# Kernel tuning notes

Hardware: AMD Instinct MI355X
Metric: run time of the kernel (lower is better)

Reference implementation:

```python
import jax, jax.numpy as jnp
import numpy as np
import random

NQUBIT = 4
NUM_CIRCUITS = 3
SEED = 1024
C64 = jnp.complex64

SINGLE = ['rx', 'ry', 'rz', 's', 't', 'p', 'u3']
DOUBLE = ['rxx', 'ryy', 'rzz', 'swap', 'cnot', 'cp', 'ch', 'cu', 'ct', 'cz']
PCOUNT = {'rx': 1, 'ry': 1, 'rz': 1, 's': 0, 't': 0, 'p': 1, 'u3': 3,
          'rxx': 1, 'ryy': 1, 'rzz': 1, 'swap': 0, 'cnot': 0, 'cp': 1,
          'ch': 0, 'cu': 3, 'ct': 0, 'cz': 0}


def build_circuits(nqubit=NQUBIT, num_circuits=NUM_CIRCUITS, seed=SEED):
    # Replays the torch module's python `random` stream (random.seed(seed))
    rng = random.Random(seed)
    circuits, off = [], 0
    for _ in range(num_circuits):
        gates = []
        for _blk in range(3):
            for i in range(nqubit):
                g = rng.choice(SINGLE)
                gates.append((g, (i,), off, PCOUNT[g])); off += PCOUNT[g]
            c, t = rng.sample(range(0, nqubit - 1), 2)
            g = rng.choice(DOUBLE)
            gates.append((g, (c, t), off, PCOUNT[g])); off += PCOUNT[g]
        circuits.append(gates)
    return circuits, off


def u3mat(th, ph, lam):
    c = jnp.cos(th * 0.5).astype(C64)
    s = jnp.sin(th * 0.5).astype(C64)
    eip = jnp.exp(1j * ph.astype(C64))
    eil = jnp.exp(1j * lam.astype(C64))
    return jnp.stack([jnp.stack([c, -eil * s]), jnp.stack([eip * s, eip * eil * c])])


def mat1(name, p):
    if name == 's':
        return jnp.array([[1, 0], [0, 1j]], C64)
    if name == 't':
        return jnp.array([[1, 0], [0, np.exp(1j * np.pi / 4)]], C64)
    if name == 'u3':
        return u3mat(p[0], p[1], p[2])
    one = jnp.ones((), C64); zero = jnp.zeros((), C64)
    if name == 'p':
        return jnp.stack([jnp.stack([one, zero]), jnp.stack([zero, jnp.exp(1j * p[0].astype(C64))])])
    h = p[0] * 0.5
    if name == 'rx':
        c = jnp.cos(h).astype(C64); s = (-1j * jnp.sin(h)).astype(C64)
        return jnp.stack([jnp.stack([c, s]), jnp.stack([s, c])])
    if name == 'ry':
        c = jnp.cos(h).astype(C64); s = jnp.sin(h).astype(C64)
        return jnp.stack([jnp.stack([c, -s]), jnp.stack([s, c])])
    if name == 'rz':
        e = jnp.exp(-1j * h.astype(C64))
        return jnp.stack([jnp.stack([e, zero]), jnp.stack([zero, jnp.conj(e)])])
    raise ValueError(name)


def mat2(name, p):
    if name == 'swap':
        return jnp.array([[1, 0, 0, 0], [0, 0, 1, 0], [0, 1, 0, 0], [0, 0, 0, 1]], C64)
    if name == 'cnot':
        return jnp.array([[1, 0, 0, 0], [0, 1, 0, 0], [0, 0, 0, 1], [0, 0, 1, 0]], C64)
    if name == 'cz':
        return jnp.diag(jnp.array([1, 1, 1, -1], C64))
    if name == 'ct':
        return jnp.diag(jnp.array([1, 1, 1, np.exp(1j * np.pi / 4)], C64))
    if name == 'ch':
        m = np.eye(4, dtype=np.complex64); r = 1.0 / np.sqrt(2.0)
        m[2:, 2:] = [[r, r], [r, -r]]
        return jnp.asarray(m)
    if name == 'cp':
        one = jnp.ones((), C64)
        return jnp.diag(jnp.stack([one, one, one, jnp.exp(1j * p[0].astype(C64))]))
    if name == 'cu':
        return jnp.zeros((4, 4), C64).at[:2, :2].set(jnp.eye(2, dtype=C64)).at[2:, 2:].set(u3mat(p[0], p[1], p[2]))
    h = p[0] * 0.5
    if name == 'rzz':
        e = jnp.exp(-1j * h.astype(C64)); ec = jnp.conj(e)
        return jnp.diag(jnp.stack([e, ec, ec, e]))
    if name == 'rxx':
        c = jnp.cos(h).astype(C64); s = (-1j * jnp.sin(h)).astype(C64)
        XX = jnp.array([[0, 0, 0, 1], [0, 0, 1, 0], [0, 1, 0, 0], [1, 0, 0, 0]], C64)
        return c * jnp.eye(4, dtype=C64) + s * XX
    if name == 'ryy':
        c = jnp.cos(h).astype(C64); s = (1j * jnp.sin(h)).astype(C64)
        YY = jnp.array([[0, 0, 0, 1], [0, 0, -1, 0], [0, -1, 0, 0], [1, 0, 0, 0]], C64)
        return c * jnp.eye(4, dtype=C64) + s * YY
    raise ValueError(name)


def apply1(state, U, q):
    # state: (N, 2,2,2,2); contract qubit-q axis with U
    state = jnp.moveaxis(state, 1 + q, -1)
    state = state @ U.T
    return jnp.moveaxis(state, -1, 1 + q)


def apply2(state, U, q0, q1):
    state = jnp.moveaxis(state, (1 + q0, 1 + q1), (-2, -1))
    sh = state.shape
    state = (state.reshape(sh[:-2] + (4,)) @ U.T).reshape(sh)
    return jnp.moveaxis(state, (-2, -1), (1 + q0, 1 + q1))


def zsigns(nqubit):
    idx = np.arange(2 ** nqubit)
    return np.stack([1.0 - 2.0 * ((idx >> (nqubit - 1 - q)) & 1) for q in range(nqubit)]).astype(np.float32)


def run_circuit(angles, params, gates, nqubit):
    N = angles.shape[0]
    h = angles * 0.5
    # rx(angle)|0> = [cos(a/2), -i sin(a/2)] per qubit -> product state (encode layer)
    v = jnp.stack([jnp.cos(h), -1j * jnp.sin(h)], axis=-1).astype(C64)  # (N, nq, 2)
    state = jnp.ones((N,), C64)
    for i in range(nqubit):
        state = state[..., None] * v[:, i].reshape((N,) + (1,) * i + (2,))
    for (name, qs, off, cnt) in gates:
        p = params[off:off + cnt]
        if len(qs) == 1:
            state = apply1(state, mat1(name, p), qs[0])
        else:
            state = apply2(state, mat2(name, p), qs[0], qs[1])
    probs = (state.real ** 2 + state.imag ** 2).reshape(N, -1)
    return probs @ jnp.asarray(zsigns(nqubit)).T  # (N, nqubit) Pauli-Z expectations


def _forward(x, params):
    B, C, H, W = x.shape
    circuits, _ = build_circuits()
    x_unf = jnp.moveaxis(x.reshape(B, C, H // 2, 2, W), 3, 4)  # torch unfold(2, 2, 2)
    xr = x_unf.reshape(-1, NQUBIT)
    exps = [run_circuit(xr, params, g, NQUBIT) for g in circuits]
    return jnp.stack(exps, axis=1).reshape(B, NUM_CIRCUITS, W, W)


def setup_inputs():
    key = jax.random.key(0)
    k1, k2 = jax.random.split(key)
    x = jax.random.normal(k1, (512, 1, 64, 64), jnp.float32)
    _, nparams = build_circuits()
    params = jax.random.uniform(k2, (nparams,), jnp.float32, -np.pi, np.pi)
    return {"x": x, "params": params}


def reference(x, params):
    return _forward(x, params)
```

## Files before the change

kernel.cpp:

```cpp
#include <hip/hip_runtime.h>
#include <stdint.h>


namespace {

typedef _Float16 half8 __attribute__((ext_vector_type(8)));
typedef _Float16 half4 __attribute__((ext_vector_type(4)));
typedef float float4v __attribute__((ext_vector_type(4)));

struct GateList {
  int ty[45];
  int q0[45];
  int q1[45];
  int off[45];
};

struct PyRandom {
  uint32_t mt[624];
  int mti;
  void init_genrand(uint32_t s) {
    mt[0] = s;
    for (int i = 1; i < 624; ++i)
      mt[i] = 1812433253u * (mt[i - 1] ^ (mt[i - 1] >> 30)) + (uint32_t)i;
    mti = 624;
  }
  void init_by_array(const uint32_t* key, int klen) {
    init_genrand(19650218u);
    int i = 1, j = 0;
    int k = 624 > klen ? 624 : klen;
    for (; k; --k) {
      mt[i] = (mt[i] ^ ((mt[i - 1] ^ (mt[i - 1] >> 30)) * 1664525u)) + key[j] + (uint32_t)j;
      ++i; ++j;
      if (i >= 624) { mt[0] = mt[623]; i = 1; }
      if (j >= klen) j = 0;
    }
    for (k = 623; k; --k) {
      mt[i] = (mt[i] ^ ((mt[i - 1] ^ (mt[i - 1] >> 30)) * 1566083941u)) - (uint32_t)i;
      ++i;
      if (i >= 624) { mt[0] = mt[623]; i = 1; }
    }
    mt[0] = 0x80000000u;
    mti = 624;
  }
  uint32_t genrand() {
    if (mti >= 624) {
      const uint32_t mag[2] = {0u, 0x9908b0dfu};
      int kk; uint32_t y;
      for (kk = 0; kk < 227; ++kk) {
        y = (mt[kk] & 0x80000000u) | (mt[kk + 1] & 0x7fffffffu);
        mt[kk] = mt[kk + 397] ^ (y >> 1) ^ mag[y & 1];
      }
      for (; kk < 623; ++kk) {
        y = (mt[kk] & 0x80000000u) | (mt[kk + 1] & 0x7fffffffu);
        mt[kk] = mt[kk - 227] ^ (y >> 1) ^ mag[y & 1];
      }
      y = (mt[623] & 0x80000000u) | (mt[0] & 0x7fffffffu);
      mt[623] = mt[396] ^ (y >> 1) ^ mag[y & 1];
      mti = 0;
    }
    uint32_t y = mt[mti++];
    y ^= y >> 11;
    y ^= (y << 7) & 0x9d2c5680u;
    y ^= (y << 15) & 0xefc60000u;
    y ^= y >> 18;
    return y;
  }
  uint32_t getrandbits(int k) { return genrand() >> (32 - k); }
  uint32_t randbelow(uint32_t n) {
    int k = 32 - __builtin_clz(n);
    uint32_t r = getrandbits(k);
    while (r >= n) r = getrandbits(k);
    return r;
  }
};

void build_gatelist(GateList& gl) {
  PyRandom rng;
  uint32_t key = 1024u;
  rng.init_by_array(&key, 1);
  static const int PC_S[7]  = {1, 1, 1, 0, 0, 1, 3};
  static const int PC_D[10] = {1, 1, 1, 0, 0, 1, 0, 3, 0, 0};
  int off = 0, idx = 0;
  for (int circ = 0; circ < 3; ++circ) {
    for (int blk = 0; blk < 3; ++blk) {
      for (int i = 0; i < 4; ++i) {
        int g = (int)rng.randbelow(7);
        gl.ty[idx] = g; gl.q0[idx] = i; gl.q1[idx] = 0; gl.off[idx] = off;
        off += PC_S[g]; ++idx;
      }
      int pool[3] = {0, 1, 2};
      int j0 = (int)rng.randbelow(3); int c = pool[j0]; pool[j0] = pool[2];
      int j1 = (int)rng.randbelow(2); int t = pool[j1];
      int g = (int)rng.randbelow(10);
      gl.ty[idx] = 10 + g; gl.q0[idx] = c; gl.q1[idx] = t; gl.off[idx] = off;
      off += PC_D[g]; ++idx;
    }
  }
}

__device__ inline float2 cmul(float2 a, float2 b) {
  return make_float2(a.x * b.x - a.y * b.y, a.x * b.y + a.y * b.x);
}
__device__ inline float2 cadd(float2 a, float2 b) {
  return make_float2(a.x + b.x, a.y + b.y);
}
__device__ inline float2 shflx(float2 v, int m) {
  return make_float2(__shfl_xor(v.x, m), __shfl_xor(v.y, m));
}

__global__ __launch_bounds__(768) void build_T(
    const float* __restrict__ params, _Float16* __restrict__ Tws, GateList gl) {
  __shared__ float2 ldsU[768];
  __shared__ float  ldsA[3072];

  const int tid = threadIdx.x;

  ((uint64_t*)Tws)[tid] = 0ull;

  {
    const int circ = tid >> 8;
    const int col  = (tid >> 4) & 15;
    const int k    = tid & 15;

    float2 s = make_float2(k == col ? 1.f : 0.f, 0.f);

    for (int g = 0; g < 15; ++g) {
      int gi = circ * 15 + g;
      int ty = gl.ty[gi];
      int o  = gl.off[gi];
      if (ty < 7) {
        float2 G00 = make_float2(1, 0), G01 = make_float2(0, 0),
               G10 = make_float2(0, 0), G11 = make_float2(1, 0);
        if (ty == 0) {
          float c, sn; __sincosf(params[o] * 0.5f, &sn, &c);
          G00 = make_float2(c, 0); G01 = make_float2(0, -sn);
          G10 = make_float2(0, -sn); G11 = make_float2(c, 0);
        } else if (ty == 1) {
          float c, sn; __sincosf(params[o] * 0.5f, &sn, &c);
          G00 = make_float2(c, 0); G01 = make_float2(-sn, 0);
          G10 = make_float2(sn, 0); G11 = make_float2(c, 0);
        } else if (ty == 2) {
          float c, sn; __sincosf(params[o] * 0.5f, &sn, &c);
          G00 = make_float2(c, -sn); G11 = make_float2(c, sn);
        } else if (ty == 3) {
          G11 = make_float2(0, 1);
        } else if (ty == 4) {
          G11 = make_float2(0.7071067811865476f, 0.7071067811865476f);
        } else if (ty == 5) {
          float cp, sp; __sincosf(params[o], &sp, &cp);
          G11 = make_float2(cp, sp);
        } else {
          float th = params[o], phv = params[o + 1], lm = params[o + 2];
          float c, sn; __sincosf(th * 0.5f, &sn, &c);
          float cp, sp; __sincosf(phv, &sp, &cp);
          float cl, sl; __sincosf(lm, &sl, &cl);
          G00 = make_float2(c, 0);
          G01 = make_float2(-cl * sn, -sl * sn);
          G10 = make_float2(cp * sn, sp * sn);
          G11 = make_float2((cp * cl - sp * sl) * c, (cp * sl + sp * cl) * c);
        }
        int m = 1 << (3 - gl.q0[gi]);
        bool hib = (k & m) != 0;
        float2 p = shflx(s, m);
        float2 A = hib ? G11 : G00;
        float2 B = hib ? G10 : G01;
        s = cadd(cmul(A, s), cmul(B, p));
      } else {
        float2 G[4][4];
#pragma unroll
        for (int r2 = 0; r2 < 4; ++r2)
#pragma unroll
          for (int c2 = 0; c2 < 4; ++c2) G[r2][c2] = make_float2(0, 0);
        if (ty == 10) {
          float c, sn; __sincosf(params[o] * 0.5f, &sn, &c);
          G[0][0] = G[1][1] = G[2][2] = G[3][3] = make_float2(c, 0);
          G[0][3] = G[1][2] = G[2][1] = G[3][0] = make_float2(0, -sn);
        } else if (ty == 11) {
          float c, sn; __sincosf(params[o] * 0.5f, &sn, &c);
          G[0][0] = G[1][1] = G[2][2] = G[3][3] = make_float2(c, 0);
          G[0][3] = G[3][0] = make_float2(0, sn);
          G[1][2] = G[2][1] = make_float2(0, -sn);
        } else if (ty == 12) {
          float c, sn; __sincosf(params[o] * 0.5f, &sn, &c);
          G[0][0] = G[3][3] = make_float2(c, -sn);
          G[1][1] = G[2][2] = make_float2(c, sn);
        } else if (ty == 13) {
          G[0][0] = make_float2(1, 0); G[1][2] = make_float2(1, 0);
          G[2][1] = make_float2(1, 0); G[3][3] = make_float2(1, 0);
        } else if (ty == 14) {
          G[0][0] = G[1][1] = make_float2(1, 0);
          G[2][3] = G[3][2] = make_float2(1, 0);
        } else if (ty == 15) {
          G[0][0] = G[1][1] = G[2][2] = make_float2(1, 0);
          float cp, sp; __sincosf(params[o], &sp, &cp);
          G[3][3] = make_float2(cp, sp);
        } else if (ty == 16) {
          G[0][0] = G[1][1] = make_float2(1, 0);
          float rv = 0.7071067811865476f;
          G[2][2] = make_float2(rv, 0); G[2][3] = make_float2(rv, 0);
          G[3][2] = make_float2(rv, 0); G[3][3] = make_float2(-rv, 0);
        } else if (ty == 17) {
          G[0][0] = G[1][1] = make_float2(1, 0);
          float th = params[o], phv = params[o + 1], lm = params[o + 2];
          float c, sn; __sincosf(th * 0.5f, &sn, &c);
          float cp, sp; __sincosf(phv, &sp, &cp);
          float cl, sl; __sincosf(lm, &sl, &cl);
          G[2][2] = make_float2(c, 0);
          G[2][3] = make_float2(-cl * sn, -sl * sn);
          G[3][2] = make_float2(cp * sn, sp * sn);
          G[3][3] = make_float2((cp * cl - sp * sl) * c, (cp * sl + sp * cl) * c);
        } else if (ty == 18) {
          G[0][0] = G[1][1] = G[2][2] = make_float2(1, 0);
          G[3][3] = make_float2(0.7071067811865476f, 0.7071067811865476f);
        } else {
          G[0][0] = G[1][1] = G[2][2] = make_float2(1, 0);
          G[3][3] = make_float2(-1, 0);
        }
        int m0 = 1 << (3 - gl.q0[gi]);
        int m1 = 1 << (3 - gl.q1[gi]);
        bool b0 = (k & m0) != 0;
        bool b1 = (k & m1) != 0;
        float2 p0 = s;
        float2 p1 = shflx(s, m1);
        float2 p2 = shflx(s, m0);
        float2 p3 = shflx(s, m0 ^ m1);
        float2 acc = make_float2(0, 0);
#pragma unroll
        for (int jj = 0; jj < 4; ++jj) {
          float2 r0 = b1 ? G[1][1 ^ jj] : G[0][0 ^ jj];
          float2 r1 = b1 ? G[3][3 ^ jj] : G[2][2 ^ jj];
          float2 coef = b0 ? r1 : r0;
          float2 pj = (jj == 0) ? p0 : (jj == 1) ? p1 : (jj == 2) ? p2 : p3;
          acc = cadd(acc, cmul(coef, pj));
        }
        s = acc;
      }
    }

    int pc = __popc(col) & 3;
    float2 ph = make_float2(1, 0);
    if (pc == 1) ph = make_float2(0, -1);
    else if (pc == 2) ph = make_float2(-1, 0);
    else if (pc == 3) ph = make_float2(0, 1);
    float2 v = cmul(s, ph);

    ldsU[(circ * 16 + k) * 16 + col] = v;
  }
  __syncthreads();

  {
    const int circ = tid >> 8;
    const int k    = (tid >> 4) & 15;
    const int l    = tid & 15;
    float a0 = 0.f, a1 = 0.f, a2 = 0.f, a3 = 0.f;
#pragma unroll
    for (int i = 0; i < 16; ++i) {
      float2 uk = ldsU[(circ * 16 + i) * 16 + k];
      float2 ul = ldsU[(circ * 16 + i) * 16 + l];
      float t = uk.x * ul.x + uk.y * ul.y;
      a0 += (i & 8) ? -t : t;
      a1 += (i & 4) ? -t : t;
      a2 += (i & 2) ? -t : t;
      a3 += (i & 1) ? -t : t;
    }
    ldsA[((circ * 4 + 0) * 16 + k) * 16 + l] = a0;
    ldsA[((circ * 4 + 1) * 16 + k) * 16 + l] = a1;
    ldsA[((circ * 4 + 2) * 16 + k) * 16 + l] = a2;
    ldsA[((circ * 4 + 3) * 16 + k) * 16 + l] = a3;
  }
  __syncthreads();

  for (int idx = tid; idx < 1152; idx += 768) {
    int cq = idx / 96;
    int K  = idx - cq * 96;
    int mf = K >> 5, r = K & 31;
    if (r >= 27) continue;
    int jarr[4] = {mf, r / 9, (r / 3) % 3, r % 3};
    float acc = 0.f;
    for (int sel = 0; sel < 16; ++sel) {
      int kk = 0, ll = 0;
      float sg = 1.f;
#pragma unroll
      for (int q = 0; q < 4; ++q) {
        int t = (sel >> (3 - q)) & 1;
        kk |= t << (3 - q);
        int lb = (jarr[q] == 2) ? (1 - t) : t;
        ll |= lb << (3 - q);
        if (jarr[q] == 1 && t) sg = -sg;
      }
      acc += sg * ldsA[(cq * 16 + kk) * 16 + ll];
    }
    float T = acc * 0.0625f;
    _Float16 th = (_Float16)T;
    _Float16 tl = (_Float16)(T - (float)th);
    int L  = ((r >> 3) << 4) | cq;
    int jj = r & 7;
    Tws[((mf * 2 + 0) * 64 + L) * 8 + jj] = th;
    Tws[((mf * 2 + 1) * 64 + L) * 8 + jj] = tl;
  }
}

__global__ __launch_bounds__(256, 4) void qconv_main(
    const float* __restrict__ x, const _Float16* __restrict__ T,
    float* __restrict__ out) {
  __shared__ _Float16 lds[256 * 40];
  const int tid  = threadIdx.x;
  const int wid  = tid >> 6;
  const int lane = tid & 63;
  const int quad = lane >> 4;
  const int n16  = lane & 15;
  const int r = blockIdx.x * 256 + tid;

  const int b  = r >> 10;
  const int h2 = (r >> 5) & 31;
  const int j  = r & 31;
  const float* xb = x + b * 4096 + h2 * 128 + j * 2;
  float2 lo = *(const float2*)(xb);
  float2 hi = *(const float2*)(xb + 64);
  float c0, s0, c1, s1, c2, s2, c3, s3;
  __sincosf(lo.x, &s0, &c0);
  __sincosf(hi.x, &s1, &c1);
  __sincosf(lo.y, &s2, &c2);
  __sincosf(hi.y, &s3, &c3);

  float f1a[3] = {1.f, c1, s1};
  float f23[9];
  {
    float f2a[3] = {1.f, c2, s2}, f3a[3] = {1.f, c3, s3};
#pragma unroll
    for (int a = 0; a < 9; ++a) f23[a] = f2a[a / 3] * f3a[a % 3];
  }
  __align__(16) _Float16 gh[32];
#pragma unroll
  for (int r1 = 0; r1 < 3; ++r1)
#pragma unroll
    for (int b9 = 0; b9 < 9; ++b9)
      gh[r1 * 9 + b9] = (_Float16)(f1a[r1] * f23[b9]);
#pragma unroll
  for (int e = 27; e < 32; ++e) gh[e] = (_Float16)0.f;

  {
    half8* dst = (half8*)&lds[tid * 40];
    dst[0] = *(const half8*)&gh[0];
    dst[1] = *(const half8*)&gh[8];
    dst[2] = *(const half8*)&gh[16];
    dst[3] = *(const half8*)&gh[24];
    half4 f0h = {(_Float16)1.f, (_Float16)c0, (_Float16)s0, (_Float16)0.f};
    *(half4*)&lds[tid * 40 + 32] = f0h;
  }
  __syncthreads();

  const half8* Tv = (const half8*)T;
  half8 afh[3], afl[3];
#pragma unroll
  for (int mf = 0; mf < 3; ++mf) {
    afh[mf] = Tv[(mf * 2 + 0) * 64 + lane];
    afl[mf] = Tv[(mf * 2 + 1) * 64 + lane];
  }

  half8 slice[4];
  half4 f0v[4];
#pragma unroll
  for (int t = 0; t < 4; ++t) {
    const int row = wid * 64 + t * 16 + n16;
    slice[t] = *(const half8*)&lds[row * 40 + quad * 8];
    f0v[t]   = *(const half4*)&lds[row * 40 + 32];
  }

  float4v acc[4];
#pragma unroll
  for (int t = 0; t < 4; ++t) acc[t] = (float4v){0.f, 0.f, 0.f, 0.f};
#pragma unroll
  for (int mf = 0; mf < 3; ++mf) {
#pragma unroll
    for (int t = 0; t < 4; ++t) {
      _Float16 f0s = f0v[t][mf];
      half8 bf;
#pragma unroll
      for (int e = 0; e < 8; ++e) bf[e] = slice[t][e] * f0s;
      acc[t] = __builtin_amdgcn_mfma_f32_16x16x32_f16(afl[mf], bf, acc[t], 0, 0, 0);
      acc[t] = __builtin_amdgcn_mfma_f32_16x16x32_f16(afh[mf], bf, acc[t], 0, 0, 0);
    }
  }

  if (quad < 3) {
#pragma unroll
    for (int t = 0; t < 4; ++t) {
      int rowg = blockIdx.x * 256 + wid * 64 + t * 16 + n16;
      float4v ev = acc[t];
      __builtin_nontemporal_store(ev, (float4v*)(out + (size_t)rowg * 12 + quad * 4));
    }
  }
}

}

extern "C" void kernel_launch(void* const* d_in, const int* in_sizes, int n_in,
                              void* d_out, int out_size, void* d_ws, size_t ws_size,
                              hipStream_t stream) {
  const float* x      = (const float*)d_in[0];
  const float* params = (const float*)d_in[1];
  float* out = (float*)d_out;
  _Float16* Tws = (_Float16*)d_ws;

  GateList gl;
  build_gatelist(gl);

  hipLaunchKernelGGL(build_T, dim3(1), dim3(768), 0, stream, params, Tws, gl);

  int nrows = in_sizes[0] / 4;
  int grid  = nrows / 256;
  hipLaunchKernelGGL(qconv_main, dim3(grid), dim3(256), 0, stream,
                     x, Tws, out);
}
```

Baseline: 80.63 us.

## Fuse transfer-matrix build into main kernel, recomputing per block in LDS

Removes the separate single-block build_T launch and its global workspace round-trip. Each block of the fused kernel rebuilds the per-circuit transfer matrix in shared memory, prefetching its x inputs before the build, then runs the MFMA contraction over 1024 rows in two passes. The LDS layout for the input features is XOR-swizzled to reduce bank conflicts. The cost is redundant matrix construction in all 512 blocks and a larger shared-memory footprint per block, which may limit occupancy.

```diff
diff --git a/kernel.cpp b/kernel.cpp
--- a/kernel.cpp
+++ b/kernel.cpp
@@ -108,169 +108,197 @@
   return make_float2(__shfl_xor(v.x, m), __shfl_xor(v.y, m));
 }
 
-__global__ __launch_bounds__(768) void build_T(
-    const float* __restrict__ params, _Float16* __restrict__ Tws, GateList gl) {
-  __shared__ float2 ldsU[768];
-  __shared__ float  ldsA[3072];
+__global__ __launch_bounds__(512, 4) void qconv_fused(
+    const float* __restrict__ x, const float* __restrict__ params,
+    float* __restrict__ out, GateList gl, int nP) {
+  __shared__ __align__(16) char smem[47104];
+  _Float16* ldsG = (_Float16*)smem;
+  float2*   ldsU = (float2*)smem;
+  float*    ldsA = (float*)(smem + 6144);
+  float*    ldsP = (float*)(smem + 18432);
+  _Float16* ldsT = (_Float16*)(smem + 40960);
 
   const int tid = threadIdx.x;
-
-  ((uint64_t*)Tws)[tid] = 0ull;
+  const int bid = blockIdx.x;
 
   {
-    const int circ = tid >> 8;
-    const int col  = (tid >> 4) & 15;
-    const int k    = tid & 15;
-
-    float2 s = make_float2(k == col ? 1.f : 0.f, 0.f);
-
-    for (int g = 0; g < 15; ++g) {
-      int gi = circ * 15 + g;
-      int ty = gl.ty[gi];
-      int o  = gl.off[gi];
-      if (ty < 7) {
-        float2 G00 = make_float2(1, 0), G01 = make_float2(0, 0),
-               G10 = make_float2(0, 0), G11 = make_float2(1, 0);
-        if (ty == 0) {
-          float c, sn; __sincosf(params[o] * 0.5f, &sn, &c);
-          G00 = make_float2(c, 0); G01 = make_float2(0, -sn);
-          G10 = make_float2(0, -sn); G11 = make_float2(c, 0);
-        } else if (ty == 1) {
-          float c, sn; __sincosf(params[o] * 0.5f, &sn, &c);
-          G00 = make_float2(c, 0); G01 = make_float2(-sn, 0);
-          G10 = make_float2(sn, 0); G11 = make_float2(c, 0);
-        } else if (ty == 2) {
-          float c, sn; __sincosf(params[o] * 0.5f, &sn, &c);
-          G00 = make_float2(c, -sn); G11 = make_float2(c, sn);
-        } else if (ty == 3) {
-          G11 = make_float2(0, 1);
-        } else if (ty == 4) {
-          G11 = make_float2(0.7071067811865476f, 0.7071067811865476f);
-        } else if (ty == 5) {
-          float cp, sp; __sincosf(params[o], &sp, &cp);
-          G11 = make_float2(cp, sp);
+    uint64_t* z = (uint64_t*)ldsT;
+    for (int i = tid; i < 768; i += 512) z[i] = 0;
+  }
+  for (int i = tid; i < nP; i += 512) ldsP[i] = params[i];
+
+  float2 plo[2], phi[2];
+#pragma unroll
+  for (int t2 = 0; t2 < 2; ++t2) {
+    int r = bid * 1024 + t2 * 512 + tid;
+    const float* xb = x + ((r >> 10) << 12) + (((r >> 5) & 31) << 7) + ((r & 31) << 1);
+    plo[t2] = *(const float2*)(xb);
+    phi[t2] = *(const float2*)(xb + 64);
+  }
+  __syncthreads();
+
+#pragma unroll
+  for (int it = 0; it < 2; ++it) {
+    int s = tid + (it << 9);
+    if (s < 768) {
+      const int circ = __builtin_amdgcn_readfirstlane(s >> 8);
+      const int col  = (s >> 4) & 15;
+      const int k    = s & 15;
+
+      float2 st = make_float2(k == col ? 1.f : 0.f, 0.f);
+
+      for (int g = 0; g < 15; ++g) {
+        int gi = circ * 15 + g;
+        int ty = gl.ty[gi];
+        int o  = gl.off[gi];
+        if (ty < 7) {
+          float2 G00 = make_float2(1, 0), G01 = make_float2(0, 0),
+                 G10 = make_float2(0, 0), G11 = make_float2(1, 0);
+          if (ty == 0) {
+            float c, sn; __sincosf(ldsP[o] * 0.5f, &sn, &c);
+            G00 = make_float2(c, 0); G01 = make_float2(0, -sn);
+            G10 = make_float2(0, -sn); G11 = make_float2(c, 0);
+          } else if (ty == 1) {
+            float c, sn; __sincosf(ldsP[o] * 0.5f, &sn, &c);
+            G00 = make_float2(c, 0); G01 = make_float2(-sn, 0);
+            G10 = make_float2(sn, 0); G11 = make_float2(c, 0);
+          } else if (ty == 2) {
+            float c, sn; __sincosf(ldsP[o] * 0.5f, &sn, &c);
+            G00 = make_float2(c, -sn); G11 = make_float2(c, sn);
+          } else if (ty == 3) {
+            G11 = make_float2(0, 1);
+          } else if (ty == 4) {
+            G11 = make_float2(0.7071067811865476f, 0.7071067811865476f);
+          } else if (ty == 5) {
+            float cp, sp; __sincosf(ldsP[o], &sp, &cp);
+            G11 = make_float2(cp, sp);
+          } else {
+            float th = ldsP[o], phv = ldsP[o + 1], lm = ldsP[o + 2];
+            float c, sn; __sincosf(th * 0.5f, &sn, &c);
+            float cp, sp; __sincosf(phv, &sp, &cp);
+            float cl, sl; __sincosf(lm, &sl, &cl);
+            G00 = make_float2(c, 0);
+            G01 = make_float2(-cl * sn, -sl * sn);
+            G10 = make_float2(cp * sn, sp * sn);
+            G11 = make_float2((cp * cl - sp * sl) * c, (cp * sl + sp * cl) * c);
+          }
+          int m = 1 << (3 - gl.q0[gi]);
+          bool hib = (k & m) != 0;
+          float2 p = shflx(st, m);
+          float2 A = hib ? G11 : G00;
+          float2 B = hib ? G10 : G01;
+          st = cadd(cmul(A, st), cmul(B, p));
         } else {
-          float th = params[o], phv = params[o + 1], lm = params[o + 2];
-          float c, sn; __sincosf(th * 0.5f, &sn, &c);
-          float cp, sp; __sincosf(phv, &sp, &cp);
-          float cl, sl; __sincosf(lm, &sl, &cl);
-          G00 = make_float2(c, 0);
-          G01 = make_float2(-cl * sn, -sl * sn);
-          G10 = make_float2(cp * sn, sp * sn);
-          G11 = make_float2((cp * cl - sp * sl) * c, (cp * sl + sp * cl) * c);
+          float2 G[4][4];
+#pragma unroll
+          for (int r2 = 0; r2 < 4; ++r2)
+#pragma unroll
+            for (int c2 = 0; c2 < 4; ++c2) G[r2][c2] = make_float2(0, 0);
+          if (ty == 10) {
+            float c, sn; __sincosf(ldsP[o] * 0.5f, &sn, &c);
+            G[0][0] = G[1][1] = G[2][2] = G[3][3] = make_float2(c, 0);
+            G[0][3] = G[1][2] = G[2][1] = G[3][0] = make_float2(0, -sn);
+          } else if (ty == 11) {
+            float c, sn; __sincosf(ldsP[o] * 0.5f, &sn, &c);
+            G[0][0] = G[1][1] = G[2][2] = G[3][3] = make_float2(c, 0);
+            G[0][3] = G[3][0] = make_float2(0, sn);
+            G[1][2] = G[2][1] = make_float2(0, -sn);
+          } else if (ty == 12) {
+            float c, sn; __sincosf(ldsP[o] * 0.5f, &sn, &c);
+            G[0][0] = G[3][3] = make_float2(c, -sn);
+            G[1][1] = G[2][2] = make_float2(c, sn);
+          } else if (ty == 13) {
+            G[0][0] = make_float2(1, 0); G[1][2] = make_float2(1, 0);
+            G[2][1] = make_float2(1, 0); G[3][3] = make_float2(1, 0);
+          } else if (ty == 14) {
+            G[0][0] = G[1][1] = make_float2(1, 0);
+            G[2][3] = G[3][2] = make_float2(1, 0);
+          } else if (ty == 15) {
+            G[0][0] = G[1][1] = G[2][2] = make_float2(1, 0);
+            float cp, sp; __sincosf(ldsP[o], &sp, &cp);
+            G[3][3] = make_float2(cp, sp);
+          } else if (ty == 16) {
+            G[0][0] = G[1][1] = make_float2(1, 0);
+            float rv = 0.7071067811865476f;
+            G[2][2] = make_float2(rv, 0); G[2][3] = make_float2(rv, 0);
+            G[3][2] = make_float2(rv, 0); G[3][3] = make_float2(-rv, 0);
+          } else if (ty == 17) {
+            G[0][0] = G[1][1] = make_float2(1, 0);
+            float th = ldsP[o], phv = ldsP[o + 1], lm = ldsP[o + 2];
+            float c, sn; __sincosf(th * 0.5f, &sn, &c);
+            float cp, sp; __sincosf(phv, &sp, &cp);
+            float cl, sl; __sincosf(lm, &sl, &cl);
+            G[2][2] = make_float2(c, 0);
+            G[2][3] = make_float2(-cl * sn, -sl * sn);
+            G[3][2] = make_float2(cp * sn, sp * sn);
+            G[3][3] = make_float2((cp * cl - sp * sl) * c, (cp * sl + sp * cl) * c);
+          } else if (ty == 18) {
+            G[0][0] = G[1][1] = G[2][2] = make_float2(1, 0);
+            G[3][3] = make_float2(0.7071067811865476f, 0.7071067811865476f);
+          } else {
+            G[0][0] = G[1][1] = G[2][2] = make_float2(1, 0);
+            G[3][3] = make_float2(-1, 0);
+          }
+          int m0 = 1 << (3 - gl.q0[gi]);
+          int m1 = 1 << (3 - gl.q1[gi]);
+          bool b0 = (k & m0) != 0;
+          bool b1 = (k & m1) != 0;
+          float2 p0 = st;
+          float2 p1 = shflx(st, m1);
+          float2 p2 = shflx(st, m0);
+          float2 p3 = shflx(st, m0 ^ m1);
+          float2 acc = make_float2(0, 0);
+#pragma unroll
+          for (int jj = 0; jj < 4; ++jj) {
+            float2 r0 = b1 ? G[1][1 ^ jj] : G[0][0 ^ jj];
+            float2 r1 = b1 ? G[3][3 ^ jj] : G[2][2 ^ jj];
+            float2 coef = b0 ? r1 : r0;
+            float2 pj = (jj == 0) ? p0 : (jj == 1) ? p1 : (jj == 2) ? p2 : p3;
+            acc = cadd(acc, cmul(coef, pj));
+          }
+          st = acc;
         }
-        int m = 1 << (3 - gl.q0[gi]);
-        bool hib = (k & m) != 0;
-        float2 p = shflx(s, m);
-        float2 A = hib ? G11 : G00;
-        float2 B = hib ? G10 : G01;
-        s = cadd(cmul(A, s), cmul(B, p));
-      } else {
-        float2 G[4][4];
-#pragma unroll
-        for (int r2 = 0; r2 < 4; ++r2)
-#pragma unroll
-          for (int c2 = 0; c2 < 4; ++c2) G[r2][c2] = make_float2(0, 0);
-        if (ty == 10) {
-          float c, sn; __sincosf(params[o] * 0.5f, &sn, &c);
-          G[0][0] = G[1][1] = G[2][2] = G[3][3] = make_float2(c, 0);
-          G[0][3] = G[1][2] = G[2][1] = G[3][0] = make_float2(0, -sn);
-        } else if (ty == 11) {
-          float c, sn; __sincosf(params[o] * 0.5f, &sn, &c);
-          G[0][0] = G[1][1] = G[2][2] = G[3][3] = make_float2(c, 0);
-          G[0][3] = G[3][0] = make_float2(0, sn);
-          G[1][2] = G[2][1] = make_float2(0, -sn);
-        } else if (ty == 12) {
-          float c, sn; __sincosf(params[o] * 0.5f, &sn, &c);
-          G[0][0] = G[3][3] = make_float2(c, -sn);
-          G[1][1] = G[2][2] = make_float2(c, sn);
-        } else if (ty == 13) {
-          G[0][0] = make_float2(1, 0); G[1][2] = make_float2(1, 0);
-          G[2][1] = make_float2(1, 0); G[3][3] = make_float2(1, 0);
-        } else if (ty == 14) {
-          G[0][0] = G[1][1] = make_float2(1, 0);
-          G[2][3] = G[3][2] = make_float2(1, 0);
-        } else if (ty == 15) {
-          G[0][0] = G[1][1] = G[2][2] = make_float2(1, 0);
-          float cp, sp; __sincosf(params[o], &sp, &cp);
-          G[3][3] = make_float2(cp, sp);
-        } else if (ty == 16) {
-          G[0][0] = G[1][1] = make_float2(1, 0);
-          float rv = 0.7071067811865476f;
-          G[2][2] = make_float2(rv, 0); G[2][3] = make_float2(rv, 0);
-          G[3][2] = make_float2(rv, 0); G[3][3] = make_float2(-rv, 0);
-        } else if (ty == 17) {
-          G[0][0] = G[1][1] = make_float2(1, 0);
-          float th = params[o], phv = params[o + 1], lm = params[o + 2];
-          float c, sn; __sincosf(th * 0.5f, &sn, &c);
-          float cp, sp; __sincosf(phv, &sp, &cp);
-          float cl, sl; __sincosf(lm, &sl, &cl);
-          G[2][2] = make_float2(c, 0);
-          G[2][3] = make_float2(-cl * sn, -sl * sn);
-          G[3][2] = make_float2(cp * sn, sp * sn);
-          G[3][3] = make_float2((cp * cl - sp * sl) * c, (cp * sl + sp * cl) * c);
-        } else if (ty == 18) {
-          G[0][0] = G[1][1] = G[2][2] = make_float2(1, 0);
-          G[3][3] = make_float2(0.7071067811865476f, 0.7071067811865476f);
-        } else {
-          G[0][0] = G[1][1] = G[2][2] = make_float2(1, 0);
-          G[3][3] = make_float2(-1, 0);
-        }
-        int m0 = 1 << (3 - gl.q0[gi]);
-        int m1 = 1 << (3 - gl.q1[gi]);
-        bool b0 = (k & m0) != 0;
-        bool b1 = (k & m1) != 0;
-        float2 p0 = s;
-        float2 p1 = shflx(s, m1);
-        float2 p2 = shflx(s, m0);
-        float2 p3 = shflx(s, m0 ^ m1);
-        float2 acc = make_float2(0, 0);
-#pragma unroll
-        for (int jj = 0; jj < 4; ++jj) {
-          float2 r0 = b1 ? G[1][1 ^ jj] : G[0][0 ^ jj];
-          float2 r1 = b1 ? G[3][3 ^ jj] : G[2][2 ^ jj];
-          float2 coef = b0 ? r1 : r0;
-          float2 pj = (jj == 0) ? p0 : (jj == 1) ? p1 : (jj == 2) ? p2 : p3;
-          acc = cadd(acc, cmul(coef, pj));
-        }
-        s = acc;
-      }
-    }
-
-    int pc = __popc(col) & 3;
-    float2 ph = make_float2(1, 0);
-    if (pc == 1) ph = make_float2(0, -1);
-    else if (pc == 2) ph = make_float2(-1, 0);
-    else if (pc == 3) ph = make_float2(0, 1);
-    float2 v = cmul(s, ph);
-
-    ldsU[(circ * 16 + k) * 16 + col] = v;
+      }
+
+      int pc = __popc(col) & 3;
+      float2 ph = make_float2(1, 0);
+      if (pc == 1) ph = make_float2(0, -1);
+      else if (pc == 2) ph = make_float2(-1, 0);
+      else if (pc == 3) ph = make_float2(0, 1);
+      float2 v = cmul(st, ph);
+
+      ldsU[(circ * 16 + k) * 16 + col] = v;
+    }
   }
   __syncthreads();
 
-  {
-    const int circ = tid >> 8;
-    const int k    = (tid >> 4) & 15;
-    const int l    = tid & 15;
-    float a0 = 0.f, a1 = 0.f, a2 = 0.f, a3 = 0.f;
-#pragma unroll
-    for (int i = 0; i < 16; ++i) {
-      float2 uk = ldsU[(circ * 16 + i) * 16 + k];
-      float2 ul = ldsU[(circ * 16 + i) * 16 + l];
-      float t = uk.x * ul.x + uk.y * ul.y;
-      a0 += (i & 8) ? -t : t;
-      a1 += (i & 4) ? -t : t;
-      a2 += (i & 2) ? -t : t;
-      a3 += (i & 1) ? -t : t;
-    }
-    ldsA[((circ * 4 + 0) * 16 + k) * 16 + l] = a0;
-    ldsA[((circ * 4 + 1) * 16 + k) * 16 + l] = a1;
-    ldsA[((circ * 4 + 2) * 16 + k) * 16 + l] = a2;
-    ldsA[((circ * 4 + 3) * 16 + k) * 16 + l] = a3;
+#pragma unroll
+  for (int it = 0; it < 2; ++it) {
+    int s = tid + (it << 9);
+    if (s < 768) {
+      const int circ = s >> 8;
+      const int k    = (s >> 4) & 15;
+      const int l    = s & 15;
+      float a0 = 0.f, a1 = 0.f, a2 = 0.f, a3 = 0.f;
+#pragma unroll
+      for (int i = 0; i < 16; ++i) {
+        float2 uk = ldsU[(circ * 16 + i) * 16 + k];
+        float2 ul = ldsU[(circ * 16 + i) * 16 + l];
+        float t = uk.x * ul.x + uk.y * ul.y;
+        a0 += (i & 8) ? -t : t;
+        a1 += (i & 4) ? -t : t;
+        a2 += (i & 2) ? -t : t;
+        a3 += (i & 1) ? -t : t;
+      }
+      ldsA[((circ * 4 + 0) * 16 + k) * 16 + l] = a0;
+      ldsA[((circ * 4 + 1) * 16 + k) * 16 + l] = a1;
+      ldsA[((circ * 4 + 2) * 16 + k) * 16 + l] = a2;
+      ldsA[((circ * 4 + 3) * 16 + k) * 16 + l] = a3;
+    }
   }
   __syncthreads();
 
-  for (int idx = tid; idx < 1152; idx += 768) {
+  for (int idx = tid; idx < 1152; idx += 512) {
     int cq = idx / 96;
     int K  = idx - cq * 96;
     int mf = K >> 5, r = K & 31;
@@ -290,67 +318,22 @@
       }
       acc += sg * ldsA[(cq * 16 + kk) * 16 + ll];
     }
-    float T = acc * 0.0625f;
-    _Float16 th = (_Float16)T;
-    _Float16 tl = (_Float16)(T - (float)th);
+    float Tval = acc * 0.0625f;
+    _Float16 th = (_Float16)Tval;
+    _Float16 tl = (_Float16)(Tval - (float)th);
     int L  = ((r >> 3) << 4) | cq;
     int jj = r & 7;
-    Tws[((mf * 2 + 0) * 64 + L) * 8 + jj] = th;
-    Tws[((mf * 2 + 1) * 64 + L) * 8 + jj] = tl;
-  }
-}
-
-__global__ __launch_bounds__(256, 4) void qconv_main(
-    const float* __restrict__ x, const _Float16* __restrict__ T,
-    float* __restrict__ out) {
-  __shared__ _Float16 lds[256 * 40];
-  const int tid  = threadIdx.x;
+    ldsT[((mf * 2 + 0) * 64 + L) * 8 + jj] = th;
+    ldsT[((mf * 2 + 1) * 64 + L) * 8 + jj] = tl;
+  }
+  __syncthreads();
+
   const int wid  = tid >> 6;
   const int lane = tid & 63;
   const int quad = lane >> 4;
   const int n16  = lane & 15;
-  const int r = blockIdx.x * 256 + tid;
-
-  const int b  = r >> 10;
-  const int h2 = (r >> 5) & 31;
-  const int j  = r & 31;
-  const float* xb = x + b * 4096 + h2 * 128 + j * 2;
-  float2 lo = *(const float2*)(xb);
-  float2 hi = *(const float2*)(xb + 64);
-  float c0, s0, c1, s1, c2, s2, c3, s3;
-  __sincosf(lo.x, &s0, &c0);
-  __sincosf(hi.x, &s1, &c1);
-  __sincosf(lo.y, &s2, &c2);
-  __sincosf(hi.y, &s3, &c3);
-
-  float f1a[3] = {1.f, c1, s1};
-  float f23[9];
-  {
-    float f2a[3] = {1.f, c2, s2}, f3a[3] = {1.f, c3, s3};
-#pragma unroll
-    for (int a = 0; a < 9; ++a) f23[a] = f2a[a / 3] * f3a[a % 3];
-  }
-  __align__(16) _Float16 gh[32];
-#pragma unroll
-  for (int r1 = 0; r1 < 3; ++r1)
-#pragma unroll
-    for (int b9 = 0; b9 < 9; ++b9)
-      gh[r1 * 9 + b9] = (_Float16)(f1a[r1] * f23[b9]);
-#pragma unroll
-  for (int e = 27; e < 32; ++e) gh[e] = (_Float16)0.f;
-
-  {
-    half8* dst = (half8*)&lds[tid * 40];
-    dst[0] = *(const half8*)&gh[0];
-    dst[1] = *(const half8*)&gh[8];
-    dst[2] = *(const half8*)&gh[16];
-    dst[3] = *(const half8*)&gh[24];
-    half4 f0h = {(_Float16)1.f, (_Float16)c0, (_Float16)s0, (_Float16)0.f};
-    *(half4*)&lds[tid * 40 + 32] = f0h;
-  }
-  __syncthreads();
-
-  const half8* Tv = (const half8*)T;
+
+  const half8* Tv = (const half8*)ldsT;
   half8 afh[3], afl[3];
 #pragma unroll
   for (int mf = 0; mf < 3; ++mf) {
@@ -358,38 +341,77 @@
     afl[mf] = Tv[(mf * 2 + 1) * 64 + lane];
   }
 
-  half8 slice[4];
-  half4 f0v[4];
-#pragma unroll
-  for (int t = 0; t < 4; ++t) {
-    const int row = wid * 64 + t * 16 + n16;
-    slice[t] = *(const half8*)&lds[row * 40 + quad * 8];
-    f0v[t]   = *(const half4*)&lds[row * 40 + 32];
-  }
-
-  float4v acc[4];
-#pragma unroll
-  for (int t = 0; t < 4; ++t) acc[t] = (float4v){0.f, 0.f, 0.f, 0.f};
-#pragma unroll
-  for (int mf = 0; mf < 3; ++mf) {
+#pragma unroll 1
+  for (int t2 = 0; t2 < 2; ++t2) {
+    float c0, s0, c1, s1, c2, s2, c3, s3;
+    __sincosf(plo[t2].x, &s0, &c0);
+    __sincosf(phi[t2].x, &s1, &c1);
+    __sincosf(plo[t2].y, &s2, &c2);
+    __sincosf(phi[t2].y, &s3, &c3);
+
+    float f1a[3] = {1.f, c1, s1};
+    float f23[9];
+    {
+      float f2a[3] = {1.f, c2, s2}, f3a[3] = {1.f, c3, s3};
+#pragma unroll
+      for (int a = 0; a < 9; ++a) f23[a] = f2a[a / 3] * f3a[a % 3];
+    }
+    __align__(16) _Float16 gh[32];
+#pragma unroll
+    for (int r1 = 0; r1 < 3; ++r1)
+#pragma unroll
+      for (int b9 = 0; b9 < 9; ++b9)
+        gh[r1 * 9 + b9] = (_Float16)(f1a[r1] * f23[b9]);
+#pragma unroll
+    for (int e = 27; e < 32; ++e) gh[e] = (_Float16)0.f;
+
+    {
+      half8* dst = (half8*)&ldsG[tid * 40];
+      int wkey = (tid >> 3) & 3;
+      dst[0 ^ wkey] = *(const half8*)&gh[0];
+      dst[1 ^ wkey] = *(const half8*)&gh[8];
+      dst[2 ^ wkey] = *(const half8*)&gh[16];
+      dst[3 ^ wkey] = *(const half8*)&gh[24];
+      half4 f0h = {(_Float16)1.f, (_Float16)c0, (_Float16)s0, (_Float16)0.f};
+      *(half4*)&ldsG[tid * 40 + 32] = f0h;
+    }
+    __syncthreads();
+
+    half8 slice[4];
+    half4 f0v[4];
 #pragma unroll
     for (int t = 0; t < 4; ++t) {
-      _Float16 f0s = f0v[t][mf];
-      half8 bf;
-#pragma unroll
-      for (int e = 0; e < 8; ++e) bf[e] = slice[t][e] * f0s;
-      acc[t] = __builtin_amdgcn_mfma_f32_16x16x32_f16(afl[mf], bf, acc[t], 0, 0, 0);
-      acc[t] = __builtin_amdgcn_mfma_f32_16x16x32_f16(afh[mf], bf, acc[t], 0, 0, 0);
-    }
-  }
-
-  if (quad < 3) {
-#pragma unroll
-    for (int t = 0; t < 4; ++t) {
-      int rowg = blockIdx.x * 256 + wid * 64 + t * 16 + n16;
-      float4v ev = acc[t];
-      __builtin_nontemporal_store(ev, (float4v*)(out + (size_t)rowg * 12 + quad * 4));
-    }
+      const int row = wid * 64 + t * 16 + n16;
+      const int rkey = (row >> 3) & 3;
+      slice[t] = *(const half8*)&ldsG[row * 40 + ((quad ^ rkey) << 3)];
+      f0v[t]   = *(const half4*)&ldsG[row * 40 + 32];
+    }
+
+    float4v acc[4];
+#pragma unroll
+    for (int t = 0; t < 4; ++t) acc[t] = (float4v){0.f, 0.f, 0.f, 0.f};
+#pragma unroll
+    for (int mf = 0; mf < 3; ++mf) {
+#pragma unroll
+      for (int t = 0; t < 4; ++t) {
+        _Float16 f0s = f0v[t][mf];
+        half8 bf;
+#pragma unroll
+        for (int e = 0; e < 8; ++e) bf[e] = slice[t][e] * f0s;
+        acc[t] = __builtin_amdgcn_mfma_f32_16x16x32_f16(afl[mf], bf, acc[t], 0, 0, 0);
+        acc[t] = __builtin_amdgcn_mfma_f32_16x16x32_f16(afh[mf], bf, acc[t], 0, 0, 0);
+      }
+    }
+
+    if (quad < 3) {
+#pragma unroll
+      for (int t = 0; t < 4; ++t) {
+        int rowg = bid * 1024 + t2 * 512 + wid * 64 + t * 16 + n16;
+        float4v ev = acc[t];
+        __builtin_nontemporal_store(ev, (float4v*)(out + (size_t)rowg * 12 + quad * 4));
+      }
+    }
+    if (t2 == 0) __syncthreads();
   }
 }
 
@@ -401,15 +423,16 @@
   const float* x      = (const float*)d_in[0];
   const float* params = (const float*)d_in[1];
   float* out = (float*)d_out;
-  _Float16* Tws = (_Float16*)d_ws;
+  (void)d_ws; (void)ws_size;
 
   GateList gl;
   build_gatelist(gl);
 
-  hipLaunchKernelGGL(build_T, dim3(1), dim3(768), 0, stream, params, Tws, gl);
+  int nP = in_sizes[1];
+  if (nP > 160) nP = 160;
 
   int nrows = in_sizes[0] / 4;
-  int grid  = nrows / 256;
-  hipLaunchKernelGGL(qconv_main, dim3(grid), dim3(256), 0, stream,
-                     x, Tws, out);
-}
+  int grid  = nrows / 1024;
+  hipLaunchKernelGGL(qconv_fused, dim3(grid), dim3(512), 0, stream,
+                     x, params, out, gl, nP);
+}
```

New measurement: 86.56 us. +7.4%, slower.
